# Optimization experiments

Hardware: AMD Instinct MI355X
Metric: run time of the kernel (lower is better)

Reference implementation:

```python
import jax, jax.numpy as jnp
import numpy as np

N_NODE = 10000
E = 320000
E_LINK = 1280000
D = 128            # emb_input_dim = n_factors*delta_d = hid_dim
EDGE_FEAT = 24     # 2 + ceil(64/3)
SEQ = 64
K = 3


def _propagate(x, src, dst, w, n_seg):
    # out[d] = sum_{e: dst[e]=d} w[e] * x[src[e]]  (sparse matvec via gather-scatter)
    return jax.ops.segment_sum(w[:, None] * x[src], dst, num_segments=n_seg)


def setup_inputs() -> dict:
    key = jax.random.key(0)
    ks = jax.random.split(key, 16)
    inp = {
        "h_entity": jax.random.normal(ks[0], (SEQ, N_NODE, D), dtype=jnp.float32),
        "x_link": jax.random.normal(ks[1], (E, EDGE_FEAT), dtype=jnp.float32),
        "edge_weight_link": jax.random.uniform(ks[2], (E_LINK,), dtype=jnp.float32),
        "edge_index_link": jax.random.randint(ks[3], (2, E_LINK), 0, E, dtype=jnp.int32),
        "edge_index": jax.random.randint(ks[4], (2, E), 0, N_NODE, dtype=jnp.int32),
    }
    s = 0.05
    inp.update({
        "W_start": jax.random.normal(ks[5], (EDGE_FEAT, D), dtype=jnp.float32) * s,
        "b_start": jnp.zeros((D,), jnp.float32),
        "W_hl": jax.random.normal(ks[6], (K, D, D), dtype=jnp.float32) * s,
        "b_hl": jnp.zeros((D,), jnp.float32),
        "W_ec": jax.random.normal(ks[7], (D, K * 2), dtype=jnp.float32) * s,
        "b_ec": jnp.zeros((K * 2,), jnp.float32),
        "W_t": jax.random.normal(ks[8], (SEQ, 1), dtype=jnp.float32) * s,
        "b_t": jnp.zeros((1,), jnp.float32),
        "W_gcn": jax.random.normal(ks[9], (K, D, D), dtype=jnp.float32) * s,
        "b_gcn": jnp.zeros((D,), jnp.float32),
    })
    return inp


def reference(h_entity, x_link, edge_weight_link, W_start, b_start, W_hl, b_hl,
              W_ec, b_ec, W_t, b_t, W_gcn, b_gcn, edge_index_link, edge_index):
    src_l, dst_l = edge_index_link[0], edge_index_link[1]
    src_n, dst_n = edge_index[0], edge_index[1]

    # start_mlp_edge
    h_link = x_link @ W_start + b_start                      # [E, D]

    # HodgeLaguerreConv, K=3: Laguerre polynomial recurrence on edge Laplacian L
    # Tx0 = x; Tx1 = (1 - L)x; Tx_{k+1} = ((2k+1-L)Tx_k - k Tx_{k-1})/(k+1)
    Tx0 = h_link
    out_e = Tx0 @ W_hl[0]
    Tx1 = Tx0 - _propagate(Tx0, src_l, dst_l, edge_weight_link, E)
    out_e = out_e + Tx1 @ W_hl[1]
    Tx2 = (3.0 * Tx1 - _propagate(Tx1, src_l, dst_l, edge_weight_link, E) - Tx0) * 0.5
    out_e = out_e + Tx2 @ W_hl[2] + b_hl                     # [E, D]

    # per-edge causal scores, K*2 columns
    score = out_e @ W_ec + b_ec                              # [E, 2K]

    # temporal projection: [T,N,D] -> permute -> [N,D,T] @ [T,1] -> [N,D]
    h_ent = jnp.einsum('tnd,t->nd', h_entity, W_t[:, 0]) + b_t[0]

    # K-hop GCN: hop-k edge weight = softmax over the (causal, non-causal) pair k
    w_k = jax.nn.softmax(score.reshape(E, K, 2), axis=-1)[..., 0]  # [E, K]
    h = h_ent
    out_n = jnp.zeros((N_NODE, D), dtype=h_ent.dtype)
    for k in range(K):
        h = _propagate(h, src_n, dst_n, w_k[:, k], N_NODE)
        out_n = out_n + h @ W_gcn[k]
    out_n = out_n + b_gcn
    return out_n
```

## Files before the change

kernel.cpp:

```cpp
#include <hip/hip_runtime.h>

#define N_NODE   10000
#define E_EDGE   320000
#define E_LINKN  1280000
#define DIM      128
#define EFEAT    24
#define SEQLEN   64

#define SCAN_CHUNK 4096

static const size_t OFF_DEGN  = 0;
static const size_t OFF_CURN  = OFF_DEGN  + 10240*4;
static const size_t OFF_DEGL  = OFF_CURN  + 10240*4;
static const size_t OFF_CURL  = OFF_DEGL  + (size_t)E_EDGE*4;
static const size_t ZERO_BYTES= OFF_CURL  + (size_t)E_EDGE*4;
static const size_t OFF_CONST = ZERO_BYTES;
static const size_t OFF_V0    = OFF_CONST + 512*4;
static const size_t OFF_V12   = OFF_V0    + (size_t)E_EDGE*6*4;
static const size_t OFF_PW    = OFF_V12   + (size_t)E_EDGE*16*4;
static const size_t OFF_STARTN= OFF_PW    + (size_t)E_EDGE*16*4;
static const size_t OFF_SRCSN = OFF_STARTN+ 10304*4;
static const size_t OFF_POSN  = OFF_SRCSN + (size_t)E_EDGE*4;
static const size_t OFF_WKS4  = OFF_POSN  + (size_t)E_EDGE*4;
static const size_t OFF_STARTL= OFF_WKS4  + (size_t)E_EDGE*16;
static const size_t OFF_LSW   = OFF_STARTL+ ((size_t)E_EDGE+64)*4;
static const size_t OFF_HENT  = OFF_LSW   + (size_t)E_LINKN*8;
static const size_t OFF_HA    = OFF_HENT  + (size_t)N_NODE*DIM*4;
static const size_t OFF_HB    = OFF_HA    + (size_t)N_NODE*DIM*4;
static const size_t OFF_HC    = OFF_HB    + (size_t)N_NODE*DIM*4;
static const size_t OFF_PARTN = OFF_HC    + (size_t)N_NODE*DIM*4;
static const size_t OFF_PARTL = OFF_PARTN + 512*4;

__global__ void consts_kernel(const float* __restrict__ Wstart, const float* __restrict__ bstart,
                              const float* __restrict__ Whl,    const float* __restrict__ bhl,
                              const float* __restrict__ Wec,    const float* __restrict__ bec,
                              float* __restrict__ Ball, float* __restrict__ cvec) {
    __shared__ float M[128*129];
    __shared__ float sWec[768];
    __shared__ float A[768];
    int k = blockIdx.x;
    int t = threadIdx.x;

    for (int i = t; i < 768; i += 256) sWec[i] = Wec[i];

    const float* w0 = Whl;
    const float* w1 = Whl + 16384;
    const float* w2 = Whl + 32768;
    for (int idx = t; idx < 16384; idx += 256) {
        int r = idx >> 7, d = idx & 127;
        float m;
        if (k == 0)      m = w0[idx] + w1[idx] + w2[idx];
        else if (k == 1) m = -(w1[idx] + 2.f*w2[idx]);
        else             m = 0.5f * w2[idx];
        M[r*129 + d] = m;
    }
    __syncthreads();

    for (int idx = t; idx < 768; idx += 256) {
        int r = idx / 6, j = idx % 6;
        float s = 0.f;
        for (int d = 0; d < 128; d++) s += M[r*129 + d] * sWec[d*6 + j];
        A[idx] = s;
    }
    __syncthreads();

    if (t < 144) {
        int i = t / 6, j = t % 6;
        float s = 0.f;
        for (int r = 0; r < 128; r++) s += Wstart[i*128 + r] * A[r*6 + j];
        Ball[i*18 + k*6 + j] = s;
    } else if (t < 150) {
        int j = t - 144;
        float s = 0.f;
        for (int r = 0; r < 128; r++) s += bstart[r] * A[r*6 + j];
        cvec[k*6 + j] = s;
    } else if (k == 0 && t >= 160 && t < 166) {
        int j = t - 160;
        float s = bec[j];
        for (int d = 0; d < 128; d++) s += bhl[d] * sWec[d*6 + j];
        cvec[18 + j] = s;
    }
}

__global__ void v_kernel(const float* __restrict__ x, const float* __restrict__ Ball,
                         float* __restrict__ V0, float* __restrict__ V12) {
    __shared__ float sB[432];
    for (int i = threadIdx.x; i < 432; i += blockDim.x) sB[i] = Ball[i];
    __syncthreads();
    int e = blockIdx.x * blockDim.x + threadIdx.x;
    if (e >= E_EDGE) return;
    float xr[24];
    const float4* xp = (const float4*)(x + (size_t)e*24);
#pragma unroll
    for (int q = 0; q < 6; q++) {
        float4 v = xp[q];
        xr[4*q+0] = v.x; xr[4*q+1] = v.y; xr[4*q+2] = v.z; xr[4*q+3] = v.w;
    }
    float o[18];
#pragma unroll
    for (int j = 0; j < 18; j++) o[j] = 0.f;
#pragma unroll
    for (int i = 0; i < 24; i++) {
        float xv = xr[i];
#pragma unroll
        for (int j = 0; j < 18; j++) o[j] += xv * sB[i*18 + j];
    }
    float2* v0p = (float2*)(V0 + (size_t)e*6);
    v0p[0] = make_float2(o[0], o[1]);
    v0p[1] = make_float2(o[2], o[3]);
    v0p[2] = make_float2(o[4], o[5]);
    float4* v12p = (float4*)(V12 + (size_t)e*16);
    v12p[0] = make_float4(o[6],  o[7],  o[8],  o[9]);
    v12p[1] = make_float4(o[10], o[11], o[12], o[13]);
    v12p[2] = make_float4(o[14], o[15], o[16], o[17]);
}

__global__ void hist_kernel(const int* __restrict__ dst, int* __restrict__ deg, int n) {
    int e = blockIdx.x * blockDim.x + threadIdx.x;
    if (e < n) atomicAdd(deg + dst[e], 1);
}

__global__ void partial_kernel(const int* __restrict__ deg, int* __restrict__ partials, int n) {
    __shared__ int red[256];
    int b = blockIdx.x, t = threadIdx.x;
    int base = b * SCAN_CHUNK;
    int s = 0;
    for (int i = t; i < SCAN_CHUNK; i += 256) {
        int idx = base + i;
        if (idx < n) s += deg[idx];
    }
    red[t] = s;
    __syncthreads();
    for (int off = 128; off > 0; off >>= 1) {
        if (t < off) red[t] += red[t + off];
        __syncthreads();
    }
    if (t == 0) partials[b] = red[0];
}

__global__ void scan_partials_kernel(const int* __restrict__ partials, int* __restrict__ offs,
                                     int* __restrict__ start, int nb, int n) {
    __shared__ int a[256];
    int t = threadIdx.x;
    a[t] = (t < nb) ? partials[t] : 0;
    __syncthreads();
    for (int off = 1; off < 256; off <<= 1) {
        int v = (t >= off) ? a[t - off] : 0;
        __syncthreads();
        a[t] += v;
        __syncthreads();
    }
    offs[t] = (t == 0) ? 0 : a[t - 1];
    if (t == 255) start[n] = a[nb - 1];
}

__global__ void scan_block_kernel(const int* __restrict__ deg, const int* __restrict__ offs,
                                  int* __restrict__ start, int n) {
    __shared__ int s[SCAN_CHUNK];
    __shared__ int tsum[256];
    int b = blockIdx.x, t = threadIdx.x;
    int base = b * SCAN_CHUNK;
    for (int i = t; i < SCAN_CHUNK; i += 256) {
        int idx = base + i;
        s[i] = (idx < n) ? deg[idx] : 0;
    }
    __syncthreads();
    int lo = t * 16;
    int mysum = 0;
#pragma unroll
    for (int j = 0; j < 16; j++) mysum += s[lo + j];
    tsum[t] = mysum;
    __syncthreads();
    for (int off = 1; off < 256; off <<= 1) {
        int v = (t >= off) ? tsum[t - off] : 0;
        __syncthreads();
        tsum[t] += v;
        __syncthreads();
    }
    int run = offs[b] + ((t == 0) ? 0 : tsum[t - 1]);
#pragma unroll
    for (int j = 0; j < 16; j++) {
        int v = s[lo + j];
        s[lo + j] = run;
        run += v;
    }
    __syncthreads();
    for (int i = t; i < SCAN_CHUNK; i += 256) {
        int idx = base + i;
        if (idx < n) start[idx] = s[i];
    }
}

__global__ void fill_n_kernel(const int* __restrict__ srcn, const int* __restrict__ dstn,
                              const int* __restrict__ start, int* __restrict__ cursor,
                              int* __restrict__ srcs_srt, int* __restrict__ pos) {
    int e = blockIdx.x * blockDim.x + threadIdx.x;
    if (e >= E_EDGE) return;
    int d = dstn[e];
    int p = start[d] + atomicAdd(cursor + d, 1);
    srcs_srt[p] = srcn[e];
    pos[e] = p;
}

__global__ void fill_l_kernel(const int* __restrict__ srcl, const int* __restrict__ dstl,
                              const float* __restrict__ ew,
                              const int* __restrict__ start, int* __restrict__ cursor,
                              int2* __restrict__ lsw) {
    int e = blockIdx.x * blockDim.x + threadIdx.x;
    if (e >= E_LINKN) return;
    int d = dstl[e];
    int p = start[d] + atomicAdd(cursor + d, 1);
    lsw[p] = make_int2(srcl[e], __float_as_int(ew[e]));
}

__global__ void prop1_gather(const float* __restrict__ V12, const int* __restrict__ startl,
                             const int2* __restrict__ lsw, float* __restrict__ PW) {
    int e = blockIdx.x * blockDim.x + threadIdx.x;
    if (e >= E_EDGE) return;
    int s0 = startl[e], s1 = startl[e + 1];
    float acc[12];
#pragma unroll
    for (int j = 0; j < 12; j++) acc[j] = 0.f;
    float ws = 0.f;
    int2 cur = make_int2(0, 0);
    if (s0 < s1) cur = lsw[s0];
    for (int j = s0; j < s1; j++) {
        int2 nxt = (j + 1 < s1) ? lsw[j + 1] : cur;
        float w = __int_as_float(cur.y);
        const float4* vp = (const float4*)(V12 + (size_t)cur.x*16);
#pragma unroll
        for (int q = 0; q < 3; q++) {
            float4 v = vp[q];
            acc[4*q+0] += w*v.x; acc[4*q+1] += w*v.y;
            acc[4*q+2] += w*v.z; acc[4*q+3] += w*v.w;
        }
        ws += w;
        cur = nxt;
    }
    float4* pw = (float4*)(PW + (size_t)e*16);
    pw[0] = make_float4(acc[0], acc[1], acc[2],  acc[3]);
    pw[1] = make_float4(acc[4], acc[5], acc[6],  acc[7]);
    pw[2] = make_float4(acc[8], acc[9], acc[10], acc[11]);
    pw[3] = make_float4(ws, 0.f, 0.f, 0.f);
}

__global__ void prop2score_kernel(const float* __restrict__ PW,
                                  const int* __restrict__ startl, const int2* __restrict__ lsw,
                                  const float* __restrict__ V0,
                                  const float* __restrict__ cvec, const int* __restrict__ posn,
                                  float4* __restrict__ wks4) {
    __shared__ float sc[24];
    if (threadIdx.x < 24) sc[threadIdx.x] = cvec[threadIdx.x];
    __syncthreads();
    int e = blockIdx.x * blockDim.x + threadIdx.x;
    if (e >= E_EDGE) return;
    int s0 = startl[e], s1 = startl[e + 1];
    float p2[6];
#pragma unroll
    for (int j = 0; j < 6; j++) p2[j] = 0.f;
    float ws2 = 0.f;
    int2 cur = make_int2(0, 0);
    if (s0 < s1) cur = lsw[s0];
    for (int j = s0; j < s1; j++) {
        int2 nxt = (j + 1 < s1) ? lsw[j + 1] : cur;
        float w = __int_as_float(cur.y);
        const float4* pv = (const float4*)(PW + (size_t)cur.x*16);
        float4 a = pv[1];
        float4 b = pv[2];
        float4 c = pv[3];
        p2[0] += w*a.z; p2[1] += w*a.w;
        p2[2] += w*b.x; p2[3] += w*b.y; p2[4] += w*b.z; p2[5] += w*b.w;
        ws2 += w * c.x;
        cur = nxt;
    }
    const float4* pe = (const float4*)(PW + (size_t)e*16);
    float4 q0 = pe[0];
    float4 q1 = pe[1];
    float  ws1 = pe[3].x;
    float pw6[6] = {q0.x, q0.y, q0.z, q0.w, q1.x, q1.y};
    const float2* v0p = (const float2*)(V0 + (size_t)e*6);
    float2 f0 = v0p[0], f1 = v0p[1], f2 = v0p[2];
    float v0r[6] = {f0.x, f0.y, f1.x, f1.y, f2.x, f2.y};
    float S[6];
#pragma unroll
    for (int j = 0; j < 6; j++)
        S[j] = v0r[j] + pw6[j] + p2[j]
             + ws1*sc[6 + j] + ws2*sc[12 + j] + sc[j] + sc[18 + j];
    int p = posn[e];
    float w0 = 1.f / (1.f + __expf(S[1] - S[0]));
    float w1 = 1.f / (1.f + __expf(S[3] - S[2]));
    float w2 = 1.f / (1.f + __expf(S[5] - S[4]));
    wks4[p] = make_float4(w0, w1, w2, 0.f);
}

__global__ void temporal_kernel(const float4* __restrict__ h_entity, const float* __restrict__ Wt,
                                const float* __restrict__ bt, float4* __restrict__ h_ent) {
    __shared__ float sw[SEQLEN];
    if (threadIdx.x < SEQLEN) sw[threadIdx.x] = Wt[threadIdx.x];
    __syncthreads();
    int i = blockIdx.x * blockDim.x + threadIdx.x;
    if (i >= N_NODE*DIM/4) return;
    float b = bt[0];
    float4 acc = make_float4(b, b, b, b);
#pragma unroll 8
    for (int t = 0; t < SEQLEN; t++) {
        float4 v = h_entity[(size_t)t * (N_NODE*DIM/4) + i];
        float w = sw[t];
        acc.x += w*v.x; acc.y += w*v.y; acc.z += w*v.z; acc.w += w*v.w;
    }
    h_ent[i] = acc;
}

__global__ void prop_hop(const float* __restrict__ h_cur, float* __restrict__ h_next,
                         const int* __restrict__ startn, const int* __restrict__ srcs_srt,
                         const float4* __restrict__ wks4, int k) {
    int node = blockIdx.x;
    int tid  = threadIdx.x;
    int s0 = startn[node], s1 = startn[node + 1];
    float acc = 0.f;
    for (int j = s0; j < s1; j++) {
        float4 wv = wks4[j];
        float w = (k == 0) ? wv.x : (k == 1) ? wv.y : wv.z;
        int sn = srcs_srt[j];
        acc += w * h_cur[(size_t)sn*DIM + tid];
    }
    h_next[(size_t)node*DIM + tid] = acc;
}

__global__ void __launch_bounds__(256)
gemm_final(const float* __restrict__ h1, const float* __restrict__ h2,
           const float* __restrict__ h3, const float* __restrict__ Wgcn,
           const float* __restrict__ bgcn, float* __restrict__ out) {
    __shared__ float sG[128*128];
    __shared__ float sh[32*128];
    int t = threadIdx.x;
    int cg = t & 31, rg = t >> 5;
    int c0 = cg * 4, r0 = rg * 4;
    int rbase = blockIdx.x * 32;
    int nrows = N_NODE - rbase; if (nrows > 32) nrows = 32;

    float4 bb = *(const float4*)(bgcn + c0);
    float acc[4][4];
#pragma unroll
    for (int r = 0; r < 4; r++) {
        acc[r][0] = bb.x; acc[r][1] = bb.y; acc[r][2] = bb.z; acc[r][3] = bb.w;
    }

    const float* hs0[3] = {h1, h2, h3};
    for (int k = 0; k < 3; k++) {
        __syncthreads();
        const float4* gk = (const float4*)(Wgcn + (size_t)k*16384);
        float4* sg4 = (float4*)sG;
        for (int i = t; i < 4096; i += 256) sg4[i] = gk[i];
        const float4* hg = (const float4*)(hs0[k] + (size_t)rbase*128);
        float4* sh4 = (float4*)sh;
        for (int i = t; i < 1024; i += 256)
            sh4[i] = ((i >> 5) < nrows) ? hg[i] : make_float4(0.f, 0.f, 0.f, 0.f);
        __syncthreads();
#pragma unroll 2
        for (int d4 = 0; d4 < 32; d4++) {
            float4 g0 = *(const float4*)(sG + (d4*4 + 0)*128 + c0);
            float4 g1 = *(const float4*)(sG + (d4*4 + 1)*128 + c0);
            float4 g2 = *(const float4*)(sG + (d4*4 + 2)*128 + c0);
            float4 g3 = *(const float4*)(sG + (d4*4 + 3)*128 + c0);
#pragma unroll
            for (int r = 0; r < 4; r++) {
                float4 hv = *(const float4*)(sh + (r0 + r)*128 + d4*4);
                acc[r][0] += hv.x*g0.x; acc[r][1] += hv.x*g0.y; acc[r][2] += hv.x*g0.z; acc[r][3] += hv.x*g0.w;
                acc[r][0] += hv.y*g1.x; acc[r][1] += hv.y*g1.y; acc[r][2] += hv.y*g1.z; acc[r][3] += hv.y*g1.w;
                acc[r][0] += hv.z*g2.x; acc[r][1] += hv.z*g2.y; acc[r][2] += hv.z*g2.z; acc[r][3] += hv.z*g2.w;
                acc[r][0] += hv.w*g3.x; acc[r][1] += hv.w*g3.y; acc[r][2] += hv.w*g3.z; acc[r][3] += hv.w*g3.w;
            }
        }
    }
#pragma unroll
    for (int r = 0; r < 4; r++) {
        if (r0 + r < nrows)
            *(float4*)(out + (size_t)(rbase + r0 + r)*128 + c0) =
                make_float4(acc[r][0], acc[r][1], acc[r][2], acc[r][3]);
    }
}

extern "C" void kernel_launch(void* const* d_in, const int* in_sizes, int n_in,
                              void* d_out, int out_size, void* d_ws, size_t ws_size,
                              hipStream_t stream) {
    const float* h_entity = (const float*)d_in[0];
    const float* x_link   = (const float*)d_in[1];
    const float* ewl      = (const float*)d_in[2];
    const int*   eil      = (const int*)d_in[3];
    const int*   ein      = (const int*)d_in[4];
    const float* Wstart   = (const float*)d_in[5];
    const float* bstart   = (const float*)d_in[6];
    const float* Whl      = (const float*)d_in[7];
    const float* bhl      = (const float*)d_in[8];
    const float* Wec      = (const float*)d_in[9];
    const float* bec      = (const float*)d_in[10];
    const float* Wt       = (const float*)d_in[11];
    const float* bt       = (const float*)d_in[12];
    const float* Wgcn     = (const float*)d_in[13];
    const float* bgcn     = (const float*)d_in[14];
    float* out = (float*)d_out;
    char*  ws  = (char*)d_ws;

    const int* srcl = eil;
    const int* dstl = eil + E_LINKN;
    const int* srcn = ein;
    const int* dstn = ein + E_EDGE;

    int*    degn  = (int*)   (ws + OFF_DEGN);
    int*    curn  = (int*)   (ws + OFF_CURN);
    int*    degl  = (int*)   (ws + OFF_DEGL);
    int*    curl  = (int*)   (ws + OFF_CURL);
    float*  Ball  = (float*) (ws + OFF_CONST);
    float*  cvec  = Ball + 432;
    float*  V0    = (float*) (ws + OFF_V0);
    float*  V12   = (float*) (ws + OFF_V12);
    float*  PW    = (float*) (ws + OFF_PW);
    int*    startn= (int*)   (ws + OFF_STARTN);
    int*    srcsn = (int*)   (ws + OFF_SRCSN);
    int*    posn  = (int*)   (ws + OFF_POSN);
    float4* wks4  = (float4*)(ws + OFF_WKS4);
    int*    startl= (int*)   (ws + OFF_STARTL);
    int2*   lsw   = (int2*)  (ws + OFF_LSW);
    float*  h_ent = (float*) (ws + OFF_HENT);
    float*  h_a   = (float*) (ws + OFF_HA);
    float*  h_b   = (float*) (ws + OFF_HB);
    float*  h_c   = (float*) (ws + OFF_HC);
    int*    partn = (int*)   (ws + OFF_PARTN);
    int*    partl = (int*)   (ws + OFF_PARTL);

    const int nbN = (N_NODE + SCAN_CHUNK - 1) / SCAN_CHUNK;
    const int nbL = (E_EDGE + SCAN_CHUNK - 1) / SCAN_CHUNK;

    hipMemsetAsync(ws, 0, ZERO_BYTES, stream);

    consts_kernel<<<3, 256, 0, stream>>>(Wstart, bstart, Whl, bhl, Wec, bec, Ball, cvec);
    v_kernel<<<(E_EDGE + 255)/256, 256, 0, stream>>>(x_link, Ball, V0, V12);

    hist_kernel<<<(E_EDGE + 255)/256, 256, 0, stream>>>(dstn, degn, E_EDGE);
    hist_kernel<<<(E_LINKN + 255)/256, 256, 0, stream>>>(dstl, degl, E_LINKN);

    partial_kernel<<<nbN, 256, 0, stream>>>(degn, partn, N_NODE);
    scan_partials_kernel<<<1, 256, 0, stream>>>(partn, partn + 256, startn, nbN, N_NODE);
    scan_block_kernel<<<nbN, 256, 0, stream>>>(degn, partn + 256, startn, N_NODE);

    partial_kernel<<<nbL, 256, 0, stream>>>(degl, partl, E_EDGE);
    scan_partials_kernel<<<1, 256, 0, stream>>>(partl, partl + 256, startl, nbL, E_EDGE);
    scan_block_kernel<<<nbL, 256, 0, stream>>>(degl, partl + 256, startl, E_EDGE);

    fill_n_kernel<<<(E_EDGE + 255)/256, 256, 0, stream>>>(srcn, dstn, startn, curn, srcsn, posn);
    fill_l_kernel<<<(E_LINKN + 255)/256, 256, 0, stream>>>(srcl, dstl, ewl, startl, curl, lsw);

    prop1_gather<<<(E_EDGE + 255)/256, 256, 0, stream>>>(V12, startl, lsw, PW);
    prop2score_kernel<<<(E_EDGE + 255)/256, 256, 0, stream>>>(PW, startl, lsw, V0, cvec,
                                                              posn, wks4);

    temporal_kernel<<<(N_NODE*DIM/4 + 255)/256, 256, 0, stream>>>(
        (const float4*)h_entity, Wt, bt, (float4*)h_ent);

    prop_hop<<<N_NODE, DIM, 0, stream>>>(h_ent, h_a, startn, srcsn, wks4, 0);
    prop_hop<<<N_NODE, DIM, 0, stream>>>(h_a,   h_b, startn, srcsn, wks4, 1);
    prop_hop<<<N_NODE, DIM, 0, stream>>>(h_b,   h_c, startn, srcsn, wks4, 2);

    gemm_final<<<(N_NODE + 31)/32, 256, 0, stream>>>(h_a, h_b, h_c, Wgcn, bgcn, out);
}
```

Baseline: 953.7 us.

## Fuse CSR build into fewer launches and pair nodes per block in hop propagation

The separate memset is folded into the constants kernel, and both histograms are merged into the edge-projection kernel. The partial-sum kernel now finishes the partial scan in its last block through an atomic counter. The link and node scans run in one launch, and both fill passes run in one kernel that counts down the degree arrays instead of using separate cursor arrays. prop_hop now handles two nodes per 256-thread block and prefetches the next neighbour index and weight, to cut launch count and hide gather latency; edge order inside each CSR segment changes, so float summation order may differ.

```diff
diff --git a/kernel.cpp b/kernel.cpp
--- a/kernel.cpp
+++ b/kernel.cpp
@@ -8,12 +8,13 @@
 #define SEQLEN   64
 
 #define SCAN_CHUNK 4096
+#define NB_L 79
+#define NB_N 3
 
 static const size_t OFF_DEGN  = 0;
-static const size_t OFF_CURN  = OFF_DEGN  + 10240*4;
-static const size_t OFF_DEGL  = OFF_CURN  + 10240*4;
-static const size_t OFF_CURL  = OFF_DEGL  + (size_t)E_EDGE*4;
-static const size_t ZERO_BYTES= OFF_CURL  + (size_t)E_EDGE*4;
+static const size_t OFF_DEGL  = OFF_DEGN  + 10240*4;
+static const size_t OFF_DONE  = OFF_DEGL  + (size_t)E_EDGE*4;
+static const size_t ZERO_BYTES= OFF_DONE  + 256;
 static const size_t OFF_CONST = ZERO_BYTES;
 static const size_t OFF_V0    = OFF_CONST + 512*4;
 static const size_t OFF_V12   = OFF_V0    + (size_t)E_EDGE*6*4;
@@ -34,12 +35,16 @@
 __global__ void consts_kernel(const float* __restrict__ Wstart, const float* __restrict__ bstart,
                               const float* __restrict__ Whl,    const float* __restrict__ bhl,
                               const float* __restrict__ Wec,    const float* __restrict__ bec,
-                              float* __restrict__ Ball, float* __restrict__ cvec) {
+                              float* __restrict__ Ball, float* __restrict__ cvec,
+                              int4* __restrict__ zreg) {
     __shared__ float M[128*129];
     __shared__ float sWec[768];
     __shared__ float A[768];
     int k = blockIdx.x;
     int t = threadIdx.x;
+
+    for (int i = blockIdx.x*256 + t; i < (int)(ZERO_BYTES/16); i += 3*256)
+        zreg[i] = make_int4(0, 0, 0, 0);
 
     for (int i = t; i < 768; i += 256) sWec[i] = Wec[i];
 
@@ -82,13 +87,20 @@
     }
 }
 
-__global__ void v_kernel(const float* __restrict__ x, const float* __restrict__ Ball,
-                         float* __restrict__ V0, float* __restrict__ V12) {
+__global__ void v_hist_kernel(const float* __restrict__ x, const float* __restrict__ Ball,
+                              const int* __restrict__ dstl, const int* __restrict__ dstn,
+                              float* __restrict__ V0, float* __restrict__ V12,
+                              int* __restrict__ degl, int* __restrict__ degn) {
+    int e = blockIdx.x * 256 + threadIdx.x;
+    atomicAdd(degl + dstl[e], 1);
+
+    if (blockIdx.x >= 1250) return;
+    atomicAdd(degn + dstn[e], 1);
+
     __shared__ float sB[432];
-    for (int i = threadIdx.x; i < 432; i += blockDim.x) sB[i] = Ball[i];
-    __syncthreads();
-    int e = blockIdx.x * blockDim.x + threadIdx.x;
-    if (e >= E_EDGE) return;
+    for (int i = threadIdx.x; i < 432; i += 256) sB[i] = Ball[i];
+    __syncthreads();
+
     float xr[24];
     const float4* xp = (const float4*)(x + (size_t)e*24);
 #pragma unroll
@@ -115,15 +127,18 @@
     v12p[2] = make_float4(o[14], o[15], o[16], o[17]);
 }
 
-__global__ void hist_kernel(const int* __restrict__ dst, int* __restrict__ deg, int n) {
-    int e = blockIdx.x * blockDim.x + threadIdx.x;
-    if (e < n) atomicAdd(deg + dst[e], 1);
-}
-
-__global__ void partial_kernel(const int* __restrict__ deg, int* __restrict__ partials, int n) {
+__global__ void partial_scanp_kernel(const int* __restrict__ degl, const int* __restrict__ degn,
+                                     int* __restrict__ partl, int* __restrict__ partn,
+                                     int* __restrict__ done,
+                                     int* __restrict__ startl, int* __restrict__ startn) {
     __shared__ int red[256];
+    __shared__ int lastflag;
     int b = blockIdx.x, t = threadIdx.x;
-    int base = b * SCAN_CHUNK;
+
+    const int* deg; int n, base; int* part;
+    if (b < NB_L) { deg = degl; n = E_EDGE;  base = b*SCAN_CHUNK;          part = partl + b; }
+    else          { deg = degn; n = N_NODE;  base = (b-NB_L)*SCAN_CHUNK;   part = partn + (b-NB_L); }
+
     int s = 0;
     for (int i = t; i < SCAN_CHUNK; i += 256) {
         int idx = base + i;
@@ -135,31 +150,55 @@
         if (t < off) red[t] += red[t + off];
         __syncthreads();
     }
-    if (t == 0) partials[b] = red[0];
-}
-
-__global__ void scan_partials_kernel(const int* __restrict__ partials, int* __restrict__ offs,
-                                     int* __restrict__ start, int nb, int n) {
-    __shared__ int a[256];
-    int t = threadIdx.x;
-    a[t] = (t < nb) ? partials[t] : 0;
-    __syncthreads();
-    for (int off = 1; off < 256; off <<= 1) {
-        int v = (t >= off) ? a[t - off] : 0;
-        __syncthreads();
-        a[t] += v;
-        __syncthreads();
-    }
-    offs[t] = (t == 0) ? 0 : a[t - 1];
-    if (t == 255) start[n] = a[nb - 1];
-}
-
-__global__ void scan_block_kernel(const int* __restrict__ deg, const int* __restrict__ offs,
-                                  int* __restrict__ start, int n) {
+    if (t == 0) {
+        *part = red[0];
+        __threadfence();
+        lastflag = (atomicAdd(done, 1) == NB_L + NB_N - 1);
+    }
+    __syncthreads();
+    if (!lastflag) return;
+    __threadfence();
+
+    {
+        __shared__ int a[256];
+        a[t] = (t < NB_L) ? partl[t] : 0;
+        __syncthreads();
+        for (int off = 1; off < 256; off <<= 1) {
+            int v = (t >= off) ? a[t - off] : 0;
+            __syncthreads();
+            a[t] += v;
+            __syncthreads();
+        }
+        partl[256 + t] = (t == 0) ? 0 : a[t - 1];
+        if (t == 255) startl[E_EDGE] = a[NB_L - 1];
+    }
+    __syncthreads();
+    {
+        __shared__ int a2[256];
+        a2[t] = (t < NB_N) ? partn[t] : 0;
+        __syncthreads();
+        for (int off = 1; off < 256; off <<= 1) {
+            int v = (t >= off) ? a2[t - off] : 0;
+            __syncthreads();
+            a2[t] += v;
+            __syncthreads();
+        }
+        partn[256 + t] = (t == 0) ? 0 : a2[t - 1];
+        if (t == 255) startn[N_NODE] = a2[NB_N - 1];
+    }
+}
+
+__global__ void scan_block_kernel(const int* __restrict__ degl, const int* __restrict__ degn,
+                                  const int* __restrict__ partl, const int* __restrict__ partn,
+                                  int* __restrict__ startl, int* __restrict__ startn) {
     __shared__ int s[SCAN_CHUNK];
     __shared__ int tsum[256];
     int b = blockIdx.x, t = threadIdx.x;
-    int base = b * SCAN_CHUNK;
+
+    const int* deg; const int* offs; int* start; int n, base;
+    if (b < NB_L) { deg = degl; offs = partl + 256; start = startl; n = E_EDGE; base = b*SCAN_CHUNK; }
+    else { deg = degn; offs = partn + 256; start = startn; n = N_NODE; base = (b-NB_L)*SCAN_CHUNK; b -= NB_L; }
+
     for (int i = t; i < SCAN_CHUNK; i += 256) {
         int idx = base + i;
         s[i] = (idx < n) ? deg[idx] : 0;
@@ -191,26 +230,27 @@
     }
 }
 
-__global__ void fill_n_kernel(const int* __restrict__ srcn, const int* __restrict__ dstn,
-                              const int* __restrict__ start, int* __restrict__ cursor,
-                              int* __restrict__ srcs_srt, int* __restrict__ pos) {
-    int e = blockIdx.x * blockDim.x + threadIdx.x;
-    if (e >= E_EDGE) return;
-    int d = dstn[e];
-    int p = start[d] + atomicAdd(cursor + d, 1);
-    srcs_srt[p] = srcn[e];
-    pos[e] = p;
-}
-
-__global__ void fill_l_kernel(const int* __restrict__ srcl, const int* __restrict__ dstl,
-                              const float* __restrict__ ew,
-                              const int* __restrict__ start, int* __restrict__ cursor,
-                              int2* __restrict__ lsw) {
-    int e = blockIdx.x * blockDim.x + threadIdx.x;
-    if (e >= E_LINKN) return;
-    int d = dstl[e];
-    int p = start[d] + atomicAdd(cursor + d, 1);
-    lsw[p] = make_int2(srcl[e], __float_as_int(ew[e]));
+__global__ void fill_both_kernel(const int* __restrict__ srcl, const int* __restrict__ dstl,
+                                 const float* __restrict__ ewl,
+                                 const int* __restrict__ srcn, const int* __restrict__ dstn,
+                                 const int* __restrict__ startl, const int* __restrict__ startn,
+                                 int* __restrict__ degl, int* __restrict__ degn,
+                                 int2* __restrict__ lsw,
+                                 int* __restrict__ srcs_srt, int* __restrict__ posn) {
+    int e = blockIdx.x * 256 + threadIdx.x;
+    {
+        int d = dstl[e];
+        int old = atomicSub(degl + d, 1);
+        int p = startl[d] + old - 1;
+        lsw[p] = make_int2(srcl[e], __float_as_int(ewl[e]));
+    }
+    if (blockIdx.x < 1250) {
+        int d = dstn[e];
+        int old = atomicSub(degn + d, 1);
+        int p = startn[d] + old - 1;
+        srcs_srt[p] = srcn[e];
+        posn[e] = p;
+    }
 }
 
 __global__ void prop1_gather(const float* __restrict__ V12, const int* __restrict__ startl,
@@ -314,15 +354,25 @@
 __global__ void prop_hop(const float* __restrict__ h_cur, float* __restrict__ h_next,
                          const int* __restrict__ startn, const int* __restrict__ srcs_srt,
                          const float4* __restrict__ wks4, int k) {
-    int node = blockIdx.x;
-    int tid  = threadIdx.x;
+    int half = threadIdx.x >> 7;
+    int tid  = threadIdx.x & 127;
+    int node = blockIdx.x * 2 + half;
     int s0 = startn[node], s1 = startn[node + 1];
     float acc = 0.f;
+    int sn = 0; float w = 0.f;
+    if (s0 < s1) {
+        sn = srcs_srt[s0];
+        float4 wv = wks4[s0];
+        w = (k == 0) ? wv.x : (k == 1) ? wv.y : wv.z;
+    }
     for (int j = s0; j < s1; j++) {
-        float4 wv = wks4[j];
-        float w = (k == 0) ? wv.x : (k == 1) ? wv.y : wv.z;
-        int sn = srcs_srt[j];
-        acc += w * h_cur[(size_t)sn*DIM + tid];
+        int sn_c = sn; float w_c = w;
+        if (j + 1 < s1) {
+            sn = srcs_srt[j + 1];
+            float4 wv = wks4[j + 1];
+            w = (k == 0) ? wv.x : (k == 1) ? wv.y : wv.z;
+        }
+        acc += w_c * h_cur[(size_t)sn_c*DIM + tid];
     }
     h_next[(size_t)node*DIM + tid] = acc;
 }
@@ -408,9 +458,8 @@
     const int* dstn = ein + E_EDGE;
 
     int*    degn  = (int*)   (ws + OFF_DEGN);
-    int*    curn  = (int*)   (ws + OFF_CURN);
     int*    degl  = (int*)   (ws + OFF_DEGL);
-    int*    curl  = (int*)   (ws + OFF_CURL);
+    int*    done  = (int*)   (ws + OFF_DONE);
     float*  Ball  = (float*) (ws + OFF_CONST);
     float*  cvec  = Ball + 432;
     float*  V0    = (float*) (ws + OFF_V0);
@@ -429,38 +478,24 @@
     int*    partn = (int*)   (ws + OFF_PARTN);
     int*    partl = (int*)   (ws + OFF_PARTL);
 
-    const int nbN = (N_NODE + SCAN_CHUNK - 1) / SCAN_CHUNK;
-    const int nbL = (E_EDGE + SCAN_CHUNK - 1) / SCAN_CHUNK;
-
-    hipMemsetAsync(ws, 0, ZERO_BYTES, stream);
-
-    consts_kernel<<<3, 256, 0, stream>>>(Wstart, bstart, Whl, bhl, Wec, bec, Ball, cvec);
-    v_kernel<<<(E_EDGE + 255)/256, 256, 0, stream>>>(x_link, Ball, V0, V12);
-
-    hist_kernel<<<(E_EDGE + 255)/256, 256, 0, stream>>>(dstn, degn, E_EDGE);
-    hist_kernel<<<(E_LINKN + 255)/256, 256, 0, stream>>>(dstl, degl, E_LINKN);
-
-    partial_kernel<<<nbN, 256, 0, stream>>>(degn, partn, N_NODE);
-    scan_partials_kernel<<<1, 256, 0, stream>>>(partn, partn + 256, startn, nbN, N_NODE);
-    scan_block_kernel<<<nbN, 256, 0, stream>>>(degn, partn + 256, startn, N_NODE);
-
-    partial_kernel<<<nbL, 256, 0, stream>>>(degl, partl, E_EDGE);
-    scan_partials_kernel<<<1, 256, 0, stream>>>(partl, partl + 256, startl, nbL, E_EDGE);
-    scan_block_kernel<<<nbL, 256, 0, stream>>>(degl, partl + 256, startl, E_EDGE);
-
-    fill_n_kernel<<<(E_EDGE + 255)/256, 256, 0, stream>>>(srcn, dstn, startn, curn, srcsn, posn);
-    fill_l_kernel<<<(E_LINKN + 255)/256, 256, 0, stream>>>(srcl, dstl, ewl, startl, curl, lsw);
-
+    consts_kernel<<<3, 256, 0, stream>>>(Wstart, bstart, Whl, bhl, Wec, bec,
+                                         Ball, cvec, (int4*)ws);
+    v_hist_kernel<<<E_LINKN/256, 256, 0, stream>>>(x_link, Ball, dstl, dstn,
+                                                   V0, V12, degl, degn);
+    partial_scanp_kernel<<<NB_L + NB_N, 256, 0, stream>>>(degl, degn, partl, partn,
+                                                          done, startl, startn);
+    scan_block_kernel<<<NB_L + NB_N, 256, 0, stream>>>(degl, degn, partl, partn,
+                                                       startl, startn);
+    fill_both_kernel<<<E_LINKN/256, 256, 0, stream>>>(srcl, dstl, ewl, srcn, dstn,
+                                                      startl, startn, degl, degn,
+                                                      lsw, srcsn, posn);
     prop1_gather<<<(E_EDGE + 255)/256, 256, 0, stream>>>(V12, startl, lsw, PW);
     prop2score_kernel<<<(E_EDGE + 255)/256, 256, 0, stream>>>(PW, startl, lsw, V0, cvec,
                                                               posn, wks4);
-
     temporal_kernel<<<(N_NODE*DIM/4 + 255)/256, 256, 0, stream>>>(
         (const float4*)h_entity, Wt, bt, (float4*)h_ent);
-
-    prop_hop<<<N_NODE, DIM, 0, stream>>>(h_ent, h_a, startn, srcsn, wks4, 0);
-    prop_hop<<<N_NODE, DIM, 0, stream>>>(h_a,   h_b, startn, srcsn, wks4, 1);
-    prop_hop<<<N_NODE, DIM, 0, stream>>>(h_b,   h_c, startn, srcsn, wks4, 2);
-
+    prop_hop<<<N_NODE/2, 256, 0, stream>>>(h_ent, h_a, startn, srcsn, wks4, 0);
+    prop_hop<<<N_NODE/2, 256, 0, stream>>>(h_a,   h_b, startn, srcsn, wks4, 1);
+    prop_hop<<<N_NODE/2, 256, 0, stream>>>(h_b,   h_c, startn, srcsn, wks4, 2);
     gemm_final<<<(N_NODE + 31)/32, 256, 0, stream>>>(h_a, h_b, h_c, Wgcn, bgcn, out);
 }
```

After: 969.9 us. About the same (+1.7%).
